# Optimization experiments

Measured on AMD Instinct MI355X. Metric: run time of the kernel, lower is better.

## Reference

```python
import jax, jax.numpy as jnp
import numpy as np

D_MODEL = 1024
N_HEADS = 16
HEAD_DIM = D_MODEL // N_HEADS
ROPE_THETA = 10000.0


def _apply_rope(t, pos):
    # t: [B, H, S, hd]; pos: [B, S] int. Half-split (NeoX-style) rotation.
    hd = t.shape[-1]
    inv_freq = 1.0 / (ROPE_THETA ** (jnp.arange(0, hd, 2, dtype=t.dtype) / hd))  # [hd/2]
    ang = pos.astype(t.dtype)[:, None, :, None] * inv_freq  # [B, 1, S, hd/2]
    cos, sin = jnp.cos(ang), jnp.sin(ang)
    t1, t2 = t[..., 0::2], t[..., 1::2]
    r1 = t1 * cos - t2 * sin
    r2 = t1 * sin + t2 * cos
    # interleave back
    return jnp.stack([r1, r2], axis=-1).reshape(t.shape)


def setup_inputs() -> dict:
    key = jax.random.key(0)
    k1, k2, k3 = jax.random.split(key, 3)
    B, S = 4, 2048
    x = jax.random.normal(k1, (B, S, D_MODEL), dtype=jnp.float32)
    positions = jnp.broadcast_to(jnp.arange(S, dtype=jnp.int32), (B, S))
    Wqkv = jax.random.normal(k2, (3 * D_MODEL, D_MODEL), dtype=jnp.float32) * (1.0 / np.sqrt(D_MODEL))
    bqkv = jnp.zeros((3 * D_MODEL,), dtype=jnp.float32)
    Wo = jax.random.normal(k3, (D_MODEL, D_MODEL), dtype=jnp.float32) * (1.0 / np.sqrt(D_MODEL))
    bo = jnp.zeros((D_MODEL,), dtype=jnp.float32)
    return {"x": x, "positions": positions, "Wqkv": Wqkv, "bqkv": bqkv, "Wo": Wo, "bo": bo}


def reference(x, positions, Wqkv, bqkv, Wo, bo):
    B, S, D = x.shape
    # fused QKV projection (torch Linear: x @ W^T + b)
    qkv = x @ Wqkv.T + bqkv                      # [B, S, 3D]
    q, k, v = jnp.split(qkv, 3, axis=-1)
    def to_heads(t):
        return t.reshape(B, S, N_HEADS, HEAD_DIM).transpose(0, 2, 1, 3)  # [B, H, S, hd]
    q, k, v = to_heads(q), to_heads(k), to_heads(v)
    q = _apply_rope(q, positions)
    k = _apply_rope(k, positions)
    scale = 1.0 / np.sqrt(HEAD_DIM)
    scores = jnp.einsum('bhqd,bhkd->bhqk', q, k) * scale   # [B, H, S, S]
    causal = jnp.tril(jnp.ones((S, S), dtype=bool))
    scores = jnp.where(causal, scores, jnp.finfo(scores.dtype).min)
    attn = jax.nn.softmax(scores, axis=-1)
    h = jnp.einsum('bhqk,bhkd->bhqd', attn, v)             # [B, H, S, hd]
    h = h.transpose(0, 2, 1, 3).reshape(B, S, D)
    return h @ Wo.T + bo
```

## Files before the change

kernel.cpp:

```cpp
#include <hip/hip_runtime.h>

#define DEV static __device__ __forceinline__

typedef __attribute__((ext_vector_type(8))) short short8;
typedef __attribute__((ext_vector_type(4))) short short4v;
typedef __attribute__((ext_vector_type(4))) float f32x4;
typedef __attribute__((ext_vector_type(4))) unsigned short ushort4v;
typedef __attribute__((ext_vector_type(4))) float float4v;

#define DM 1024
#define NH 16
#define HD 64
#define SS 2048
#define TOK 8192

DEV unsigned short f2bf(float f) {
  union { float f; unsigned u; } v; v.f = f;
  unsigned r = v.u + 0x7FFFu + ((v.u >> 16) & 1u);
  return (unsigned short)(r >> 16);
}
DEV float bf2f(unsigned short h) {
  union { unsigned u; float f; } v; v.u = ((unsigned)h) << 16;
  return v.f;
}

#define MFMA16x32(a, b, c) __builtin_amdgcn_mfma_f32_16x16x32_bf16((a), (b), (c), 0, 0, 0)

DEV f32x4 mfma_pv(short4v a, short4v b, f32x4 c) {
#if __has_builtin(__builtin_amdgcn_mfma_f32_16x16x16bf16_1k)
  return __builtin_amdgcn_mfma_f32_16x16x16bf16_1k(a, b, c, 0, 0, 0);
#else
  f32x4 d;
  asm("v_mfma_f32_16x16x16_bf16 %0, %1, %2, %3" : "=&v"(d) : "v"(a), "v"(b), "v"(c));
  return d;
#endif
}

DEV void gload_lds16(const unsigned short* g, unsigned short* l) {
  __builtin_amdgcn_global_load_lds(
      (const __attribute__((address_space(1))) void*)g,
      (__attribute__((address_space(3))) void*)l, 16, 0, 0);
}

__global__ __launch_bounds__(256) void k_cvt(const float* __restrict__ in,
                                             unsigned short* __restrict__ out, int n4) {
  int i = blockIdx.x * 256 + threadIdx.x;
  if (i >= n4) return;
  float4v v = ((const float4v*)in)[i];
  ushort4v o;
  o[0] = f2bf(v[0]); o[1] = f2bf(v[1]); o[2] = f2bf(v[2]); o[3] = f2bf(v[3]);
  ((ushort4v*)out)[i] = o;
}

__global__ __launch_bounds__(256) void k_tab(const int* __restrict__ pos,
                                             float* __restrict__ tc, float* __restrict__ ts) {
  int i = blockIdx.x * 256 + threadIdx.x;
  int t = i >> 5, fi = i & 31;
  float p = (float)pos[t];
  float inv = powf(10000.0f, -(float)fi / 32.0f);
  float a = p * inv;
  float sv, cv;
  sincosf(a, &sv, &cv);
  tc[i] = cv;
  ts[i] = sv;
}

template <int MODE>
__global__ __launch_bounds__(512) void k_gemm3(
    const unsigned short* __restrict__ A, const unsigned short* __restrict__ Bm,
    const float* __restrict__ bias, void* __restrict__ out0, void* __restrict__ out1,
    void* __restrict__ out2, const float* __restrict__ tabc,
    const float* __restrict__ tabs, int M, int N, int K) {
  __shared__ __align__(16) unsigned short Abuf[3][256 * 64];
  __shared__ __align__(16) unsigned short Bbuf[3][128 * 64];
  const int tid = threadIdx.x;
  const int wid = tid >> 6, lane = tid & 63;
  const int l16 = lane & 15, lq = lane >> 4;
  const int wr = wid >> 1, wc = wid & 1;
  const int r8 = lane >> 3, c8 = lane & 7;
  const int NT = K >> 6;
  const int sx = l16 & 7;

  const int gx = N >> 7;
  const int nwg = gx * (M >> 8);
  const int chunk = nwg >> 3;
  const int bid = blockIdx.x;
  const int virt = (bid & 7) * chunk + (bid >> 3);
  const int m0 = (virt / gx) << 8;
  const int n0 = (virt % gx) << 7;

#define STAGE_G3(T, BSEL)                                                           \
  {                                                                                 \
    int k0_ = (T) << 6;                                                             \
    unsigned short* ab_ = Abuf[BSEL];                                               \
    unsigned short* bb_ = Bbuf[BSEL];                                               \
    _Pragma("unroll")                                                               \
    for (int i_ = 0; i_ < 4; ++i_) {                                                \
      int c_ = wid * 4 + i_;                                                        \
      gload_lds16(A + (size_t)(m0 + c_ * 8 + r8) * K + k0_ + ((c8 ^ r8) << 3),      \
                  &ab_[c_ * 512]);                                                  \
    }                                                                               \
    _Pragma("unroll")                                                               \
    for (int i_ = 0; i_ < 2; ++i_) {                                                \
      int c_ = wid * 2 + i_;                                                        \
      gload_lds16(Bm + (size_t)(n0 + c_ * 8 + r8) * K + k0_ + ((c8 ^ r8) << 3),     \
                  &bb_[c_ * 512]);                                                  \
    }                                                                               \
  }

  f32x4 acc[4][4];
#pragma unroll
  for (int i = 0; i < 4; i++)
#pragma unroll
    for (int j = 0; j < 4; j++) acc[i][j] = (f32x4){0.f, 0.f, 0.f, 0.f};

  STAGE_G3(0, 0)
  STAGE_G3(1, 1)
  asm volatile("s_waitcnt vmcnt(6)" ::: "memory");
  __builtin_amdgcn_s_barrier();
  __builtin_amdgcn_sched_barrier(0);

  int cb = 0, sb = 2;
  for (int t = 0; t < NT; ++t) {
    if (t + 2 < NT) STAGE_G3(t + 2, sb)
    const unsigned short* Ab = Abuf[cb];
    const unsigned short* Bb = Bbuf[cb];
#pragma unroll
    for (int kk = 0; kk < 2; ++kk) {
      int sw0 = ((kk * 4 + lq) ^ sx) << 3;
      short8 af[4], bfr[4];
#pragma unroll
      for (int mi = 0; mi < 4; ++mi)
        af[mi] = *(const short8*)&Ab[(wr * 64 + mi * 16 + l16) * 64 + sw0];
#pragma unroll
      for (int ni = 0; ni < 4; ++ni)
        bfr[ni] = *(const short8*)&Bb[(wc * 64 + ni * 16 + l16) * 64 + sw0];
#pragma unroll
      for (int mi = 0; mi < 4; ++mi)
#pragma unroll
        for (int ni = 0; ni < 4; ++ni)
          acc[mi][ni] = MFMA16x32(af[mi], bfr[ni], acc[mi][ni]);
    }
    if (t + 1 < NT) {
      if (t + 3 <= NT) {
        asm volatile("s_waitcnt vmcnt(6)" ::: "memory");
      } else {
        asm volatile("s_waitcnt vmcnt(0)" ::: "memory");
      }
      __builtin_amdgcn_s_barrier();
      __builtin_amdgcn_sched_barrier(0);
    }
    cb = (cb == 2) ? 0 : cb + 1;
    sb = (sb == 2) ? 0 : sb + 1;
  }
#undef STAGE_G3

  if (MODE == 0) {
    float* C = (float*)out0;
#pragma unroll
    for (int mi = 0; mi < 4; ++mi) {
      int row = m0 + wr * 64 + mi * 16 + lq * 4;
#pragma unroll
      for (int ni = 0; ni < 4; ++ni) {
        int col = n0 + wc * 64 + ni * 16 + l16;
        float bv = bias[col];
#pragma unroll
        for (int j = 0; j < 4; ++j)
          C[(size_t)(row + j) * N + col] = acc[mi][ni][j] + bv;
      }
    }
  } else {
    unsigned short* Qb = (unsigned short*)out0;
    unsigned short* Kb = (unsigned short*)out1;
    unsigned short* Vt = (unsigned short*)out2;
    int sel0 = n0 >> 10;
#pragma unroll
    for (int mi = 0; mi < 4; ++mi) {
      int row = m0 + wr * 64 + mi * 16 + lq * 4;
#pragma unroll
      for (int ni = 0; ni < 4; ++ni) {
        int col = n0 + wc * 64 + ni * 16 + l16;
        int hh = (col >> 6) & 15;
        int d = col & 63;
        float bv = bias[col];
        if (sel0 < 2) {
          unsigned short* P = sel0 ? Kb : Qb;
          int pfr = d >> 1;
          size_t p = ((size_t)((row >> 11) * NH + hh) * SS + (row & 2047)) * 64 + d;
#pragma unroll
          for (int j = 0; j < 4; ++j) {
            float val = acc[mi][ni][j] + bv;
            float part = __shfl_xor(val, 1, 64);
            int rr = row + j;
            float cv = tabc[((size_t)rr << 5) + pfr];
            float sv = tabs[((size_t)rr << 5) + pfr];
            float outv = (d & 1) ? (part * sv + val * cv)
                                 : (val * cv - part * sv);
            P[p + (size_t)j * 64] = f2bf(outv);
          }
        } else {
          size_t p = ((size_t)((row >> 11) * NH + hh) * 64 + d) * SS + (row & 2047);
          ushort4v o;
#pragma unroll
          for (int j = 0; j < 4; ++j) o[j] = f2bf(acc[mi][ni][j] + bv);
          *(ushort4v*)&Vt[p] = o;
        }
      }
    }
  }
}

__global__ __launch_bounds__(256) void k_attn(const unsigned short* __restrict__ Q,
                                              const unsigned short* __restrict__ K,
                                              const unsigned short* __restrict__ Vt,
                                              unsigned short* __restrict__ H) {
  __shared__ __align__(16) unsigned short Kbuf[2 * 4096];
  __shared__ __align__(16) unsigned short Vbuf[2 * 4096];

  int lin = blockIdx.x;
  int bh = lin & 63;
  int p = lin >> 6;
  int b = bh >> 4, h = bh & 15;
  int wid = threadIdx.x >> 6, lane = threadIdx.x & 63;
  int l16 = lane & 15, lq = lane >> 4;
  int sx = l16 & 7;
  const unsigned short* Qh = Q + (size_t)bh * SS * 64;
  const unsigned short* Kh = K + (size_t)bh * SS * 64;
  const unsigned short* Vh = Vt + (size_t)bh * 64 * SS;

  for (int seg = 0; seg < 2; ++seg) {
    int g = seg ? (31 - p) : p;
    int qbase = g * 64 + wid * 16;
    int qrow = qbase + l16;
    int ntk = g + 1;

    short8 aq[2];
    {
      const unsigned short* qp = Qh + (size_t)qrow * 64 + lq * 8;
      aq[0] = *(const short8*)qp;
      aq[1] = *(const short8*)(qp + 32);
    }
    f32x4 o[4];
#pragma unroll
    for (int i = 0; i < 4; ++i) o[i] = (f32x4){0.f, 0.f, 0.f, 0.f};
    float lsum = 0.f;

#pragma unroll
    for (int i = 0; i < 2; ++i) {
      int c = threadIdx.x + (i << 8);
      int row = c >> 3, col = ((c & 7) ^ (row & 7)) << 3;
      gload_lds16(Kh + (size_t)row * 64 + col, &Kbuf[c * 8]);
      gload_lds16(Vh + (size_t)row * SS + col, &Vbuf[c * 8]);
    }
    __syncthreads();

    int cur = 0;
    for (int kt = 0; kt < ntk; ++kt) {
      if (kt + 1 < ntk) {
        int kb1 = (kt + 1) << 6;
        int nb_ = (cur ^ 1) * 4096;
#pragma unroll
        for (int i = 0; i < 2; ++i) {
          int c = threadIdx.x + (i << 8);
          int row = c >> 3, col = ((c & 7) ^ (row & 7)) << 3;
          gload_lds16(Kh + (size_t)(kb1 + row) * 64 + col, &Kbuf[nb_ + c * 8]);
          gload_lds16(Vh + (size_t)row * SS + kb1 + col, &Vbuf[nb_ + c * 8]);
        }
      }
      int kb = kt << 6;
      const unsigned short* Kb_ = &Kbuf[cur * 4096];
      const unsigned short* Vb_ = &Vbuf[cur * 4096];

      f32x4 sacc[4];
#pragma unroll
      for (int nb = 0; nb < 4; ++nb) {
        int r = nb * 16 + l16;
        short8 bk0 = *(const short8*)&Kb_[r * 64 + ((lq ^ sx) << 3)];
        short8 bk1 = *(const short8*)&Kb_[r * 64 + (((4 | lq) ^ sx) << 3)];
        f32x4 z = (f32x4){0.f, 0.f, 0.f, 0.f};
        z = MFMA16x32(bk0, aq[0], z);
        z = MFMA16x32(bk1, aq[1], z);
        sacc[nb] = z;
      }
      float sc[4][4];
#pragma unroll
      for (int nb = 0; nb < 4; ++nb)
#pragma unroll
        for (int j = 0; j < 4; ++j) sc[nb][j] = sacc[nb][j] * 0.18033688f;
      if (kt == g) {
#pragma unroll
        for (int nb = 0; nb < 4; ++nb)
#pragma unroll
          for (int j = 0; j < 4; ++j) {
            int key = kb + nb * 16 + lq * 4 + j;
            if (key > qrow) sc[nb][j] = -1e30f;
          }
      }
      short4v pa[4];
#pragma unroll
      for (int nb = 0; nb < 4; ++nb) {
        float pv[4];
#pragma unroll
        for (int j = 0; j < 4; ++j) {
          float e;
          asm("v_exp_f32 %0, %1" : "=v"(e) : "v"(sc[nb][j]));
          lsum += e;
          pv[j] = e;
        }
        union { unsigned u[2]; short4v s4; } pk;
        asm("v_cvt_pk_bf16_f32 %0, %1, %2" : "=v"(pk.u[0]) : "v"(pv[0]), "v"(pv[1]));
        asm("v_cvt_pk_bf16_f32 %0, %1, %2" : "=v"(pk.u[1]) : "v"(pv[2]), "v"(pv[3]));
        pa[nb] = pk.s4;
      }
#pragma unroll
      for (int ni = 0; ni < 4; ++ni) {
        int row = ni * 16 + l16;
        f32x4 acc = o[ni];
#pragma unroll
        for (int nb = 0; nb < 4; ++nb) {
          int ch = (2 * nb + (lq >> 1)) ^ sx;
          short4v bv = *(const short4v*)&Vb_[row * 64 + ch * 8 + ((lq & 1) << 2)];
          acc = mfma_pv(pa[nb], bv, acc);
        }
        o[ni] = acc;
      }
      __syncthreads();
      cur ^= 1;
    }

    float red = lsum;
    red += __shfl_xor(red, 16, 64);
    red += __shfl_xor(red, 32, 64);
    float inv[4];
#pragma unroll
    for (int j = 0; j < 4; ++j) {
      int src = (lane & 48) + ((lane >> 4) & 3) * 4 + j;
      inv[j] = 1.0f / __shfl(red, src, 64);
    }
#pragma unroll
    for (int ni = 0; ni < 4; ++ni) {
      int d = h * 64 + ni * 16 + l16;
#pragma unroll
      for (int j = 0; j < 4; ++j) {
        int s = qbase + lq * 4 + j;
        H[((size_t)(b * SS + s)) * 1024 + d] = f2bf(o[ni][j] * inv[j]);
      }
    }
  }
}

extern "C" void kernel_launch(void* const* d_in, const int* in_sizes, int n_in,
                              void* d_out, int out_size, void* d_ws, size_t ws_size,
                              hipStream_t stream) {
  const float* x    = (const float*)d_in[0];
  const int*   pos  = (const int*)d_in[1];
  const float* Wqkv = (const float*)d_in[2];
  const float* bqkv = (const float*)d_in[3];
  const float* Wo   = (const float*)d_in[4];
  const float* bo   = (const float*)d_in[5];
  float* out = (float*)d_out;

  char* w = (char*)d_ws;
  unsigned short* x_bf    = (unsigned short*)(w + 0);
  unsigned short* h_bf    = x_bf;
  unsigned short* wqkv_bf = (unsigned short*)(w + 16777216);
  unsigned short* wo_bf   = (unsigned short*)(w + 23068672);
  unsigned short* Qb      = (unsigned short*)(w + 25165824);
  unsigned short* Kb      = (unsigned short*)(w + 41943040);
  unsigned short* Vt      = (unsigned short*)(w + 58720256);
  float* tabc             = (float*)(w + 75497472);
  float* tabs             = (float*)(w + 76546048);

  k_cvt<<<8192, 256, 0, stream>>>(x, x_bf, 2097152);
  k_cvt<<<3072, 256, 0, stream>>>(Wqkv, wqkv_bf, 786432);
  k_cvt<<<1024, 256, 0, stream>>>(Wo, wo_bf, 262144);
  k_tab<<<1024, 256, 0, stream>>>(pos, tabc, tabs);
  k_gemm3<1><<<768, 512, 0, stream>>>(x_bf, wqkv_bf, bqkv, Qb, Kb, Vt, tabc, tabs, TOK, 3072, DM);
  k_attn<<<1024, 256, 0, stream>>>(Qb, Kb, Vt, h_bf);
  k_gemm3<0><<<256, 512, 0, stream>>>(h_bf, wo_bf, bo, out, nullptr, nullptr, tabc, tabs, TOK, DM, DM);
}
```

Measured before the change: 194.8 us.

## Add 256x256-tile QKV GEMM with 4-stage pipeline and XCD-aware block remap

Introduces a new GEMM kernel for the QKV projection that uses 256x256 output tiles with K-steps of 32, a 4-deep LDS ring buffer fed by direct global-to-LDS loads, and a block index remap that groups tiles per XCD. The goal is more operand reuse per tile, fewer workgroups, and better latency hiding than the previous 256x128 three-stage kernel. It keeps the fused bias, RoPE and V-transpose epilogue. In exchange it uses larger accumulator register arrays, which risks pressure under launch_bounds(512,2), and it has a smaller grid of 384 blocks.

Result: slower. 230.7 us (+18.4%).

```diff
diff --git a/kernel.cpp b/kernel.cpp
--- a/kernel.cpp
+++ b/kernel.cpp
@@ -63,6 +63,143 @@
   sincosf(a, &sv, &cv);
   tc[i] = cv;
   ts[i] = sv;
+}
+
+template <int MODE>
+__global__ __launch_bounds__(512, 2) void k_gemm6(
+    const unsigned short* __restrict__ A, const unsigned short* __restrict__ Bm,
+    const float* __restrict__ bias, void* __restrict__ out0, void* __restrict__ out1,
+    void* __restrict__ out2, const float* __restrict__ tabc,
+    const float* __restrict__ tabs, int M, int N, int K) {
+  __shared__ __align__(16) unsigned short Abuf[4][8192];
+  __shared__ __align__(16) unsigned short Bbuf[4][8192];
+  const int tid = threadIdx.x;
+  const int wid = tid >> 6, lane = tid & 63;
+  const int l16 = lane & 15, lq = lane >> 4;
+  const int wm = wid >> 2, wn = wid & 3;
+  const int NT = K >> 5;
+
+  const int gx = N >> 8;
+  const int nwg = gx * (M >> 8);
+  const int chunk = nwg >> 3;
+  const int bid = blockIdx.x;
+  const int virt = (bid & 7) * chunk + (bid >> 3);
+  const int m0 = (virt / gx) << 8;
+  const int n0 = (virt % gx) << 8;
+
+#define STAGE_G6(T, BSEL)                                                        \
+  {                                                                              \
+    int k0_ = (T) << 5;                                                          \
+    unsigned short* ab_ = Abuf[BSEL];                                            \
+    unsigned short* bb_ = Bbuf[BSEL];                                            \
+    _Pragma("unroll")                                                            \
+    for (int i_ = 0; i_ < 2; ++i_) {                                             \
+      int c_ = tid + (i_ << 9);                                                  \
+      int l_ = c_ & 15, kc_ = (c_ >> 4) & 3, mf_ = c_ >> 6;                      \
+      gload_lds16(A + (size_t)(m0 + mf_ * 16 + l_) * K + k0_ + kc_ * 8,          \
+                  &ab_[c_ * 8]);                                                 \
+      gload_lds16(Bm + (size_t)(n0 + mf_ * 16 + l_) * K + k0_ + kc_ * 8,         \
+                  &bb_[c_ * 8]);                                                 \
+    }                                                                            \
+  }
+
+  f32x4 acc[8][4];
+#pragma unroll
+  for (int i = 0; i < 8; i++)
+#pragma unroll
+    for (int j = 0; j < 4; j++) acc[i][j] = (f32x4){0.f, 0.f, 0.f, 0.f};
+
+  STAGE_G6(0, 0)
+  STAGE_G6(1, 1)
+  STAGE_G6(2, 2)
+  asm volatile("s_waitcnt vmcnt(8)" ::: "memory");
+  __builtin_amdgcn_s_barrier();
+  __builtin_amdgcn_sched_barrier(0);
+
+  for (int t = 0; t < NT; ++t) {
+    const int cb = t & 3;
+    if (t + 3 < NT) { STAGE_G6(t + 3, (t + 3) & 3) }
+    const unsigned short* Ab = Abuf[cb];
+    const unsigned short* Bb = Bbuf[cb];
+    short8 af[8], bf[4];
+#pragma unroll
+    for (int mi = 0; mi < 8; ++mi)
+      af[mi] = *(const short8*)&Ab[(((wm * 8 + mi) * 4 + lq) * 16 + l16) * 8];
+#pragma unroll
+    for (int ni = 0; ni < 4; ++ni)
+      bf[ni] = *(const short8*)&Bb[(((wn * 4 + ni) * 4 + lq) * 16 + l16) * 8];
+#pragma unroll
+    for (int mi = 0; mi < 8; ++mi)
+#pragma unroll
+      for (int ni = 0; ni < 4; ++ni)
+        acc[mi][ni] = MFMA16x32(af[mi], bf[ni], acc[mi][ni]);
+    if (t + 1 < NT) {
+      if (t + 4 <= NT) {
+        asm volatile("s_waitcnt vmcnt(8)" ::: "memory");
+      } else if (t + 3 <= NT) {
+        asm volatile("s_waitcnt vmcnt(4)" ::: "memory");
+      } else {
+        asm volatile("s_waitcnt vmcnt(0)" ::: "memory");
+      }
+      __builtin_amdgcn_s_barrier();
+      __builtin_amdgcn_sched_barrier(0);
+    }
+  }
+#undef STAGE_G6
+
+  if (MODE == 0) {
+    float* C = (float*)out0;
+#pragma unroll
+    for (int mi = 0; mi < 8; ++mi) {
+      int row = m0 + wm * 128 + mi * 16 + lq * 4;
+#pragma unroll
+      for (int ni = 0; ni < 4; ++ni) {
+        int col = n0 + wn * 64 + ni * 16 + l16;
+        float bv = bias[col];
+#pragma unroll
+        for (int j = 0; j < 4; ++j)
+          C[(size_t)(row + j) * N + col] = acc[mi][ni][j] + bv;
+      }
+    }
+  } else {
+    unsigned short* Qb = (unsigned short*)out0;
+    unsigned short* Kb = (unsigned short*)out1;
+    unsigned short* Vt = (unsigned short*)out2;
+    int sel0 = n0 >> 10;
+#pragma unroll
+    for (int mi = 0; mi < 8; ++mi) {
+      int row = m0 + wm * 128 + mi * 16 + lq * 4;
+#pragma unroll
+      for (int ni = 0; ni < 4; ++ni) {
+        int col = n0 + wn * 64 + ni * 16 + l16;
+        int hh = (col >> 6) & 15;
+        int d = col & 63;
+        float bv = bias[col];
+        if (sel0 < 2) {
+          unsigned short* P = sel0 ? Kb : Qb;
+          int pfr = d >> 1;
+          size_t p = ((size_t)((row >> 11) * NH + hh) * SS + (row & 2047)) * 64 + d;
+#pragma unroll
+          for (int j = 0; j < 4; ++j) {
+            float val = acc[mi][ni][j] + bv;
+            float part = __shfl_xor(val, 1, 64);
+            int rr = row + j;
+            float cv = tabc[((size_t)rr << 5) + pfr];
+            float sv = tabs[((size_t)rr << 5) + pfr];
+            float outv = (d & 1) ? (part * sv + val * cv)
+                                 : (val * cv - part * sv);
+            P[p + (size_t)j * 64] = f2bf(outv);
+          }
+        } else {
+          size_t p = ((size_t)((row >> 11) * NH + hh) * 64 + d) * SS + (row & 2047);
+          ushort4v o;
+#pragma unroll
+          for (int j = 0; j < 4; ++j) o[j] = f2bf(acc[mi][ni][j] + bv);
+          *(ushort4v*)&Vt[p] = o;
+        }
+      }
+    }
+  }
 }
 
 template <int MODE>
@@ -375,7 +512,7 @@
   k_cvt<<<3072, 256, 0, stream>>>(Wqkv, wqkv_bf, 786432);
   k_cvt<<<1024, 256, 0, stream>>>(Wo, wo_bf, 262144);
   k_tab<<<1024, 256, 0, stream>>>(pos, tabc, tabs);
-  k_gemm3<1><<<768, 512, 0, stream>>>(x_bf, wqkv_bf, bqkv, Qb, Kb, Vt, tabc, tabs, TOK, 3072, DM);
+  k_gemm6<1><<<384, 512, 0, stream>>>(x_bf, wqkv_bf, bqkv, Qb, Kb, Vt, tabc, tabs, TOK, 3072, DM);
   k_attn<<<1024, 256, 0, stream>>>(Qb, Kb, Vt, h_bf);
   k_gemm3<0><<<256, 512, 0, stream>>>(h_bf, wo_bf, bo, out, nullptr, nullptr, tabc, tabs, TOK, DM, DM);
 }
```
